# Kernel tuning notes

Hardware: AMD Instinct MI355X
Metric: run time of the kernel (lower is better)

Reference implementation:

```python
import jax, jax.numpy as jnp
import numpy as np

B, N, E = 2, 50000, 800000
F_IN, H1, C1, C2 = 1433, 8, 8, 7
NEG_SLOPE = 0.2
EPS = 1e-16


def _gat_conv(x, edge_index, W, a_src, a_dst, b, heads, out_ch):
    # x: [N, F_in]; edge_index: [2, E] (row0 = source j, row1 = target i, PyG convention)
    n = x.shape[0]
    loops = jnp.arange(n)
    src = jnp.concatenate([edge_index[0], loops])  # add self-loops (PyG default)
    dst = jnp.concatenate([edge_index[1], loops])
    h = (x @ W).reshape(n, heads, out_ch)                       # [N, H, C]
    e_src = (h * a_src).sum(-1)                                 # [N, H]
    e_dst = (h * a_dst).sum(-1)                                 # [N, H]
    e = jax.nn.leaky_relu(e_src[src] + e_dst[dst], NEG_SLOPE)   # [E', H]
    # segment softmax over incoming edges of each destination node
    m = jax.ops.segment_max(e, dst, num_segments=n)             # [N, H]
    ex = jnp.exp(e - m[dst])
    den = jax.ops.segment_sum(ex, dst, num_segments=n)
    alpha = ex / (den[dst] + EPS)                               # [E', H]
    out = jax.ops.segment_sum(h[src] * alpha[:, :, None], dst, num_segments=n)  # [N, H, C]
    return out.reshape(n, heads * out_ch) + b


def setup_inputs() -> dict:
    key = jax.random.key(0)
    ks = jax.random.split(key, 8)
    x = jax.random.normal(ks[0], (B, N, F_IN), dtype=jnp.float32)
    edge_index = jax.random.randint(ks[1], (B, 2, E), 0, N, dtype=jnp.int64)
    s1 = 1.0 / np.sqrt(F_IN)
    s2 = 1.0 / np.sqrt(H1 * C1)
    return {
        "x": x,
        "edge_index": edge_index,
        "W1": jax.random.normal(ks[2], (F_IN, H1 * C1), dtype=jnp.float32) * s1,
        "a1_src": jax.random.normal(ks[3], (H1, C1), dtype=jnp.float32) * 0.3,
        "a1_dst": jax.random.normal(ks[4], (H1, C1), dtype=jnp.float32) * 0.3,
        "b1": jnp.zeros((H1 * C1,), dtype=jnp.float32),
        "W2": jax.random.normal(ks[5], (H1 * C1, C2), dtype=jnp.float32) * s2,
        "a2_src": jax.random.normal(ks[6], (1, C2), dtype=jnp.float32) * 0.3,
        "a2_dst": jax.random.normal(ks[7], (1, C2), dtype=jnp.float32) * 0.3,
        "b2": jnp.zeros((C2,), dtype=jnp.float32),
    }


def reference(x, edge_index, W1, a1_src, a1_dst, b1, W2, a2_src, a2_dst, b2):
    # Eval mode: dropout (p=0.6) is identity.
    def per_graph(xi, ei):
        h = _gat_conv(xi, ei, W1, a1_src, a1_dst, b1, H1, C1)   # [N, 64]
        h = jax.nn.elu(h)
        o = _gat_conv(h, ei, W2, a2_src, a2_dst, b2, 1, C2)     # [N, 7]
        return jax.nn.log_softmax(o, axis=-1)
    return jax.vmap(per_graph)(x, edge_index)
```

## Files before the change

kernel.cpp:

```cpp
#include <hip/hip_runtime.h>
#include <hip/hip_bf16.h>
#include <math.h>

#define NB 2
#define NN 50000
#define NE 800000
#define FIN 1433
#define KPAD 1440
#define HD 64
#define C2c 7
#define NCHUNK 196

typedef __attribute__((ext_vector_type(8))) short short8;
typedef __attribute__((ext_vector_type(4))) float f32x4;
typedef f32x4 __attribute__((aligned(4))) f32x4u;

static __device__ __forceinline__ float leaky(float e) { return e > 0.f ? e : 0.2f * e; }

static __device__ __forceinline__ short bf16r(float f) {
    __hip_bfloat16 h = __float2bfloat16(f);
    return *reinterpret_cast<short*>(&h);
}

__global__ __launch_bounds__(256) void w1t_kernel(const float* __restrict__ W,
                                                  short* __restrict__ Bt) {
    int i = blockIdx.x * 256 + threadIdx.x;
    if (i >= 64 * KPAD) return;
    int c = i / KPAD, k = i - c * KPAD;
    float v = (k < FIN) ? W[k * 64 + c] : 0.f;
    Bt[i] = bf16r(v);
}

__global__ __launch_bounds__(256) void gemm1_mfma(const float* __restrict__ x,
                                                  const short* __restrict__ Bt,
                                                  float* __restrict__ h1) {
    const int b = blockIdx.y;
    const int wave = threadIdx.x >> 6;
    const int lane = threadIdx.x & 63;
    const int m = lane & 15;
    const int quad = lane >> 4;
    const int row0 = blockIdx.x * 128 + wave * 32;

    const float* xb = x + (size_t)b * NN * FIN;
    float* hb = h1 + (size_t)b * NN * HD;

    int r0 = row0 + m;
    int r1 = row0 + 16 + m;
    int r0c = r0 < NN ? r0 : NN - 1;
    int r1c = r1 < NN ? r1 : NN - 1;
    const float* a0p = xb + (size_t)r0c * FIN + quad * 8;
    const float* a1p = xb + (size_t)r1c * FIN + quad * 8;
    const short* btp = Bt + quad * 8 + (size_t)m * KPAD;

    f32x4 acc[2][4];
#pragma unroll
    for (int t = 0; t < 2; t++)
#pragma unroll
        for (int n = 0; n < 4; n++) acc[t][n] = (f32x4){0.f, 0.f, 0.f, 0.f};

    for (int kt = 0; kt < 1408; kt += 32) {
        f32x4 af00 = *(const f32x4u*)(a0p + kt);
        f32x4 af01 = *(const f32x4u*)(a0p + kt + 4);
        f32x4 af10 = *(const f32x4u*)(a1p + kt);
        f32x4 af11 = *(const f32x4u*)(a1p + kt + 4);
        short8 fa0, fa1;
        fa0[0] = bf16r(af00[0]); fa0[1] = bf16r(af00[1]); fa0[2] = bf16r(af00[2]); fa0[3] = bf16r(af00[3]);
        fa0[4] = bf16r(af01[0]); fa0[5] = bf16r(af01[1]); fa0[6] = bf16r(af01[2]); fa0[7] = bf16r(af01[3]);
        fa1[0] = bf16r(af10[0]); fa1[1] = bf16r(af10[1]); fa1[2] = bf16r(af10[2]); fa1[3] = bf16r(af10[3]);
        fa1[4] = bf16r(af11[0]); fa1[5] = bf16r(af11[1]); fa1[6] = bf16r(af11[2]); fa1[7] = bf16r(af11[3]);
#pragma unroll
        for (int n = 0; n < 4; n++) {
            short8 fb = *(const short8*)(btp + (size_t)n * 16 * KPAD + kt);
            acc[0][n] = __builtin_amdgcn_mfma_f32_16x16x32_bf16(fa0, fb, acc[0][n], 0, 0, 0);
            acc[1][n] = __builtin_amdgcn_mfma_f32_16x16x32_bf16(fa1, fb, acc[1][n], 0, 0, 0);
        }
    }
    {
        short8 fa0, fa1;
#pragma unroll
        for (int j = 0; j < 8; j++) {
            int k = 1408 + quad * 8 + j;
            fa0[j] = bf16r(k < FIN ? a0p[1408 + j] : 0.f);
            fa1[j] = bf16r(k < FIN ? a1p[1408 + j] : 0.f);
        }
#pragma unroll
        for (int n = 0; n < 4; n++) {
            short8 fb = *(const short8*)(btp + (size_t)n * 16 * KPAD + 1408);
            acc[0][n] = __builtin_amdgcn_mfma_f32_16x16x32_bf16(fa0, fb, acc[0][n], 0, 0, 0);
            acc[1][n] = __builtin_amdgcn_mfma_f32_16x16x32_bf16(fa1, fb, acc[1][n], 0, 0, 0);
        }
    }
#pragma unroll
    for (int t = 0; t < 2; t++) {
#pragma unroll
        for (int r = 0; r < 4; r++) {
            int row = row0 + t * 16 + quad * 4 + r;
            if (row < NN) {
#pragma unroll
                for (int n = 0; n < 4; n++) hb[(size_t)row * HD + n * 16 + m] = acc[t][n][r];
            }
        }
    }
}

__global__ void coef1_kernel(const float* __restrict__ h1, const float* __restrict__ a_src,
                             const float* __restrict__ a_dst, float* __restrict__ es,
                             float* __restrict__ ed) {
    int i = blockIdx.x * blockDim.x + threadIdx.x;
    if (i >= NB * NN * 8) return;
    int h = i & 7;
    int n = i >> 3;
    const float* hp = h1 + (size_t)n * 64 + h * 8;
    float s = 0.f, d = 0.f;
#pragma unroll
    for (int c = 0; c < 8; c++) {
        float v = hp[c];
        s += v * a_src[h * 8 + c];
        d += v * a_dst[h * 8 + c];
    }
    es[i] = s;
    ed[i] = d;
}

__global__ void deg_kernel(const int* __restrict__ ei, int* __restrict__ deg) {
    int i = blockIdx.x * blockDim.x + threadIdx.x;
    if (i >= NB * NE) return;
    int b = i / NE, e = i - b * NE;
    int dst = ei[(size_t)b * 2 * NE + NE + e];
    atomicAdd(deg + b * NN + dst, 1);
}

__global__ __launch_bounds__(256) void scan1_kernel(const int* __restrict__ deg,
                                                    int* __restrict__ rowptr,
                                                    int* __restrict__ bsum) {
    const int b = blockIdx.y, th = threadIdx.x;
    const int i = blockIdx.x * 256 + th;
    __shared__ int s[256];
    int v = (i < NN) ? deg[b * NN + i] : 0;
    s[th] = v;
    __syncthreads();
    int val = v;
    for (int off = 1; off < 256; off <<= 1) {
        int t = (th >= off) ? s[th - off] : 0;
        __syncthreads();
        val += t;
        s[th] = val;
        __syncthreads();
    }
    if (i < NN) rowptr[b * (NN + 1) + i] = val - v;
    if (th == 255) bsum[b * NCHUNK + blockIdx.x] = val;
}

__global__ __launch_bounds__(256) void scan2_kernel(const int* __restrict__ bsum,
                                                    int* __restrict__ boff,
                                                    int* __restrict__ rowptr) {
    const int b = blockIdx.x, th = threadIdx.x;
    __shared__ int s[256];
    int v = (th < NCHUNK) ? bsum[b * NCHUNK + th] : 0;
    s[th] = v;
    __syncthreads();
    int val = v;
    for (int off = 1; off < 256; off <<= 1) {
        int t = (th >= off) ? s[th - off] : 0;
        __syncthreads();
        val += t;
        s[th] = val;
        __syncthreads();
    }
    if (th < NCHUNK) boff[b * NCHUNK + th] = val - v;
    if (th == 255) rowptr[b * (NN + 1) + NN] = val;
}

__global__ __launch_bounds__(256) void scan3_kernel(const int* __restrict__ boff,
                                                    int* __restrict__ rowptr,
                                                    int* __restrict__ cursor) {
    const int b = blockIdx.y;
    const int i = blockIdx.x * 256 + threadIdx.x;
    if (i >= NN) return;
    int r = rowptr[b * (NN + 1) + i] + boff[b * NCHUNK + blockIdx.x];
    rowptr[b * (NN + 1) + i] = r;
    cursor[b * NN + i] = r;
}

__global__ void scatter_kernel(const int* __restrict__ ei, int* __restrict__ cursor,
                               int* __restrict__ col) {
    int i = blockIdx.x * blockDim.x + threadIdx.x;
    if (i >= NB * NE) return;
    int b = i / NE, e = i - b * NE;
    int src = ei[(size_t)b * 2 * NE + e];
    int dst = ei[(size_t)b * 2 * NE + NE + e];
    int pos = atomicAdd(cursor + b * NN + dst, 1);
    col[(size_t)b * NE + pos] = src;
}

__global__ __launch_bounds__(256) void agg1_kernel(
    const float* __restrict__ h1, const float* __restrict__ es, const float* __restrict__ ed,
    const float* __restrict__ b1, const float* __restrict__ W2, const float* __restrict__ a2s,
    const float* __restrict__ a2d, const int* __restrict__ rowptr, const int* __restrict__ col,
    float* __restrict__ h2, float* __restrict__ es2, float* __restrict__ ed2) {
    int w = blockIdx.x * 4 + (threadIdx.x >> 6);
    if (w >= NB * NN) return;
    const int lane = threadIdx.x & 63;
    const int b = w / NN;
    const int n = w - b * NN;
    const int head = lane >> 3;
    const size_t nb = (size_t)b * NN;

    const float edv = ed[(nb + n) * 8 + head];
    float accv = 0.f, den = 0.f;
    {
        float e = leaky(es[(nb + n) * 8 + head] + edv);
        float wv = __expf(e);
        den += wv;
        accv += wv * h1[(nb + n) * 64 + lane];
    }
    const int* cp = col + (size_t)b * NE;
    const int start = rowptr[b * (NN + 1) + n];
    const int end = rowptr[b * (NN + 1) + n + 1];
    for (int idx = start; idx < end; idx++) {
        int src = cp[idx];
        float e = leaky(es[(nb + src) * 8 + head] + edv);
        float wv = __expf(e);
        den += wv;
        accv += wv * h1[(nb + src) * 64 + lane];
    }
    float o = accv / (den + 1e-16f) + b1[lane];
    float g = o > 0.f ? o : expm1f(o);

    float h2reg = 0.f;
#pragma unroll
    for (int c2 = 0; c2 < 7; c2++) {
        float v = g * W2[lane * 7 + c2];
#pragma unroll
        for (int off = 1; off < 64; off <<= 1) v += __shfl_xor(v, off, 64);
        if (lane == c2) h2reg = v;
    }
    if (lane < 8) h2[(nb + n) * 8 + lane] = (lane < 7) ? h2reg : 0.f;

    float p = (lane < 7) ? h2reg * a2s[lane] : 0.f;
#pragma unroll
    for (int off = 1; off < 64; off <<= 1) p += __shfl_xor(p, off, 64);
    float q = (lane < 7) ? h2reg * a2d[lane] : 0.f;
#pragma unroll
    for (int off = 1; off < 64; off <<= 1) q += __shfl_xor(q, off, 64);
    if (lane == 0) {
        es2[nb + n] = p;
        ed2[nb + n] = q;
    }
}

__global__ void agg2_kernel(const float* __restrict__ h2, const float* __restrict__ es2,
                            const float* __restrict__ ed2, const float* __restrict__ b2,
                            const int* __restrict__ rowptr, const int* __restrict__ col,
                            float* __restrict__ out) {
    int i = blockIdx.x * blockDim.x + threadIdx.x;
    if (i >= NB * NN) return;
    const int b = i / NN;
    const int n = i - b * NN;
    const size_t nb = (size_t)b * NN;
    const float edv = ed2[nb + n];
    float acc0 = 0, acc1 = 0, acc2 = 0, acc3 = 0, acc4 = 0, acc5 = 0, acc6 = 0, den = 0;
    {
        float e = leaky(es2[nb + n] + edv);
        float wv = __expf(e);
        den += wv;
        const float4 u0 = *(const float4*)&h2[(nb + n) * 8];
        const float4 u1 = *(const float4*)&h2[(nb + n) * 8 + 4];
        acc0 += wv * u0.x; acc1 += wv * u0.y; acc2 += wv * u0.z; acc3 += wv * u0.w;
        acc4 += wv * u1.x; acc5 += wv * u1.y; acc6 += wv * u1.z;
    }
    const int* cp = col + (size_t)b * NE;
    const int start = rowptr[b * (NN + 1) + n];
    const int end = rowptr[b * (NN + 1) + n + 1];
    for (int idx = start; idx < end; idx++) {
        int src = cp[idx];
        float e = leaky(es2[nb + src] + edv);
        float wv = __expf(e);
        den += wv;
        const float4 u0 = *(const float4*)&h2[(nb + src) * 8];
        const float4 u1 = *(const float4*)&h2[(nb + src) * 8 + 4];
        acc0 += wv * u0.x; acc1 += wv * u0.y; acc2 += wv * u0.z; acc3 += wv * u0.w;
        acc4 += wv * u1.x; acc5 += wv * u1.y; acc6 += wv * u1.z;
    }
    float inv = 1.f / (den + 1e-16f);
    float o[7];
    o[0] = acc0 * inv + b2[0]; o[1] = acc1 * inv + b2[1]; o[2] = acc2 * inv + b2[2];
    o[3] = acc3 * inv + b2[3]; o[4] = acc4 * inv + b2[4]; o[5] = acc5 * inv + b2[5];
    o[6] = acc6 * inv + b2[6];
    float m = o[0];
#pragma unroll
    for (int c = 1; c < 7; c++) m = fmaxf(m, o[c]);
    float s = 0.f;
#pragma unroll
    for (int c = 0; c < 7; c++) s += expf(o[c] - m);
    float lse = m + logf(s);
    float* op = out + ((size_t)b * NN + n) * 7;
#pragma unroll
    for (int c = 0; c < 7; c++) op[c] = o[c] - lse;
}

extern "C" void kernel_launch(void* const* d_in, const int* in_sizes, int n_in,
                              void* d_out, int out_size, void* d_ws, size_t ws_size,
                              hipStream_t stream) {
    const float* x = (const float*)d_in[0];
    const int* ei = (const int*)d_in[1];
    const float* W1 = (const float*)d_in[2];
    const float* a1s = (const float*)d_in[3];
    const float* a1d = (const float*)d_in[4];
    const float* b1 = (const float*)d_in[5];
    const float* W2 = (const float*)d_in[6];
    const float* a2s = (const float*)d_in[7];
    const float* a2d = (const float*)d_in[8];
    const float* b2 = (const float*)d_in[9];
    float* out = (float*)d_out;

    char* ws = (char*)d_ws;
    size_t off = 0;
    auto alloc = [&](size_t bytes) {
        void* p = ws + off;
        off += (bytes + 255) & ~(size_t)255;
        return p;
    };
    float* h1 = (float*)alloc((size_t)NB * NN * 64 * 4);
    float* es1 = (float*)alloc((size_t)NB * NN * 8 * 4);
    float* ed1 = (float*)alloc((size_t)NB * NN * 8 * 4);
    float* h2 = (float*)alloc((size_t)NB * NN * 8 * 4);
    float* es2 = (float*)alloc((size_t)NB * NN * 4);
    float* ed2 = (float*)alloc((size_t)NB * NN * 4);
    int* rowptr = (int*)alloc((size_t)NB * (NN + 1) * 4);
    int* cursor = (int*)alloc((size_t)NB * NN * 4);
    int* deg = (int*)alloc((size_t)NB * NN * 4);
    int* col = (int*)alloc((size_t)NB * NE * 4);
    short* Bt = (short*)alloc((size_t)64 * KPAD * 2);
    int* bsum = (int*)alloc((size_t)NB * NCHUNK * 4);
    int* boff = (int*)alloc((size_t)NB * NCHUNK * 4);

    hipMemsetAsync(deg, 0, (size_t)NB * NN * 4, stream);

    w1t_kernel<<<(64 * KPAD + 255) / 256, 256, 0, stream>>>(W1, Bt);

    dim3 ggrid((NN + 127) / 128, NB);
    gemm1_mfma<<<ggrid, 256, 0, stream>>>(x, Bt, h1);

    coef1_kernel<<<(NB * NN * 8 + 255) / 256, 256, 0, stream>>>(h1, a1s, a1d, es1, ed1);

    deg_kernel<<<(NB * NE + 255) / 256, 256, 0, stream>>>(ei, deg);
    dim3 sgrid(NCHUNK, NB);
    scan1_kernel<<<sgrid, 256, 0, stream>>>(deg, rowptr, bsum);
    scan2_kernel<<<NB, 256, 0, stream>>>(bsum, boff, rowptr);
    scan3_kernel<<<sgrid, 256, 0, stream>>>(boff, rowptr, cursor);
    scatter_kernel<<<(NB * NE + 255) / 256, 256, 0, stream>>>(ei, cursor, col);

    agg1_kernel<<<(NB * NN + 3) / 4, 256, 0, stream>>>(h1, es1, ed1, b1, W2, a2s, a2d,
                                                       rowptr, col, h2, es2, ed2);
    agg2_kernel<<<(NB * NN + 255) / 256, 256, 0, stream>>>(h2, es2, ed2, b2, rowptr, col, out);
}
```

Measured before the change: 1.243 ms.

## Store layer-1 features as bf16 and parallelize agg1 across edges per wave

The GEMM output h1 is now stored as bf16 instead of fp32, which halves the bytes gathered per neighbor in coef1 and agg1. agg1 is restructured so that each wave's 8 lane-groups process different edges in parallel, with each lane owning one head's 8 channels via a 16-byte load. Partial sums are combined with cross-lane shuffles, and the W2 projection is reduced over 8 lanes instead of 64. This shortens the serial per-edge loop and lowers gather traffic, at the cost of bf16 rounding of the hidden features.

```diff
diff --git a/kernel.cpp b/kernel.cpp
--- a/kernel.cpp
+++ b/kernel.cpp
@@ -21,6 +21,10 @@
     __hip_bfloat16 h = __float2bfloat16(f);
     return *reinterpret_cast<short*>(&h);
 }
+static __device__ __forceinline__ float bf2f(short s) {
+    unsigned u = ((unsigned)(unsigned short)s) << 16;
+    return __uint_as_float(u);
+}
 
 __global__ __launch_bounds__(256) void w1t_kernel(const float* __restrict__ W,
                                                   short* __restrict__ Bt) {
@@ -33,7 +37,7 @@
 
 __global__ __launch_bounds__(256) void gemm1_mfma(const float* __restrict__ x,
                                                   const short* __restrict__ Bt,
-                                                  float* __restrict__ h1) {
+                                                  short* __restrict__ h1b) {
     const int b = blockIdx.y;
     const int wave = threadIdx.x >> 6;
     const int lane = threadIdx.x & 63;
@@ -42,7 +46,7 @@
     const int row0 = blockIdx.x * 128 + wave * 32;
 
     const float* xb = x + (size_t)b * NN * FIN;
-    float* hb = h1 + (size_t)b * NN * HD;
+    short* hb = h1b + (size_t)b * NN * HD;
 
     int r0 = row0 + m;
     int r1 = row0 + 16 + m;
@@ -97,24 +101,24 @@
             int row = row0 + t * 16 + quad * 4 + r;
             if (row < NN) {
 #pragma unroll
-                for (int n = 0; n < 4; n++) hb[(size_t)row * HD + n * 16 + m] = acc[t][n][r];
+                for (int n = 0; n < 4; n++) hb[(size_t)row * HD + n * 16 + m] = bf16r(acc[t][n][r]);
             }
         }
     }
 }
 
-__global__ void coef1_kernel(const float* __restrict__ h1, const float* __restrict__ a_src,
+__global__ void coef1_kernel(const short* __restrict__ h1b, const float* __restrict__ a_src,
                              const float* __restrict__ a_dst, float* __restrict__ es,
                              float* __restrict__ ed) {
     int i = blockIdx.x * blockDim.x + threadIdx.x;
     if (i >= NB * NN * 8) return;
     int h = i & 7;
     int n = i >> 3;
-    const float* hp = h1 + (size_t)n * 64 + h * 8;
+    const short8 hv = *(const short8*)(h1b + (size_t)n * 64 + h * 8);
     float s = 0.f, d = 0.f;
 #pragma unroll
     for (int c = 0; c < 8; c++) {
-        float v = hp[c];
+        float v = bf2f(hv[c]);
         s += v * a_src[h * 8 + c];
         d += v * a_dst[h * 8 + c];
     }
@@ -194,58 +198,88 @@
 }
 
 __global__ __launch_bounds__(256) void agg1_kernel(
-    const float* __restrict__ h1, const float* __restrict__ es, const float* __restrict__ ed,
+    const short* __restrict__ h1b, const float* __restrict__ es, const float* __restrict__ ed,
     const float* __restrict__ b1, const float* __restrict__ W2, const float* __restrict__ a2s,
     const float* __restrict__ a2d, const int* __restrict__ rowptr, const int* __restrict__ col,
     float* __restrict__ h2, float* __restrict__ es2, float* __restrict__ ed2) {
     int w = blockIdx.x * 4 + (threadIdx.x >> 6);
     if (w >= NB * NN) return;
     const int lane = threadIdx.x & 63;
+    const int s = lane >> 3;
+    const int cg = lane & 7;
     const int b = w / NN;
     const int n = w - b * NN;
-    const int head = lane >> 3;
     const size_t nb = (size_t)b * NN;
 
-    const float edv = ed[(nb + n) * 8 + head];
-    float accv = 0.f, den = 0.f;
-    {
-        float e = leaky(es[(nb + n) * 8 + head] + edv);
+    const float edv = ed[(nb + n) * 8 + cg];
+    float den = 0.f;
+    float acc[8];
+#pragma unroll
+    for (int j = 0; j < 8; j++) acc[j] = 0.f;
+
+    if (s == 0) {
+        float e = leaky(es[(nb + n) * 8 + cg] + edv);
         float wv = __expf(e);
-        den += wv;
-        accv += wv * h1[(nb + n) * 64 + lane];
-    }
+        den = wv;
+        const short8 hv = *(const short8*)(h1b + (nb + n) * 64 + cg * 8);
+#pragma unroll
+        for (int j = 0; j < 8; j++) acc[j] = wv * bf2f(hv[j]);
+    }
+
     const int* cp = col + (size_t)b * NE;
     const int start = rowptr[b * (NN + 1) + n];
     const int end = rowptr[b * (NN + 1) + n + 1];
-    for (int idx = start; idx < end; idx++) {
+    for (int idx = start + s; idx < end; idx += 8) {
         int src = cp[idx];
-        float e = leaky(es[(nb + src) * 8 + head] + edv);
+        float e = leaky(es[(nb + src) * 8 + cg] + edv);
         float wv = __expf(e);
         den += wv;
-        accv += wv * h1[(nb + src) * 64 + lane];
-    }
-    float o = accv / (den + 1e-16f) + b1[lane];
-    float g = o > 0.f ? o : expm1f(o);
-
-    float h2reg = 0.f;
+        const short8 hv = *(const short8*)(h1b + (nb + src) * 64 + cg * 8);
+#pragma unroll
+        for (int j = 0; j < 8; j++) acc[j] += wv * bf2f(hv[j]);
+    }
+
+#pragma unroll
+    for (int off = 8; off < 64; off <<= 1) {
+        den += __shfl_xor(den, off, 64);
+#pragma unroll
+        for (int j = 0; j < 8; j++) acc[j] += __shfl_xor(acc[j], off, 64);
+    }
+
+    const float inv = 1.f / (den + 1e-16f);
+    float g[8];
+#pragma unroll
+    for (int j = 0; j < 8; j++) {
+        float o = acc[j] * inv + b1[cg * 8 + j];
+        g[j] = o > 0.f ? o : expm1f(o);
+    }
+
+    float p[7];
 #pragma unroll
     for (int c2 = 0; c2 < 7; c2++) {
-        float v = g * W2[lane * 7 + c2];
-#pragma unroll
-        for (int off = 1; off < 64; off <<= 1) v += __shfl_xor(v, off, 64);
-        if (lane == c2) h2reg = v;
-    }
-    if (lane < 8) h2[(nb + n) * 8 + lane] = (lane < 7) ? h2reg : 0.f;
-
-    float p = (lane < 7) ? h2reg * a2s[lane] : 0.f;
-#pragma unroll
-    for (int off = 1; off < 64; off <<= 1) p += __shfl_xor(p, off, 64);
-    float q = (lane < 7) ? h2reg * a2d[lane] : 0.f;
-#pragma unroll
-    for (int off = 1; off < 64; off <<= 1) q += __shfl_xor(q, off, 64);
+        float v = 0.f;
+#pragma unroll
+        for (int j = 0; j < 8; j++) v += g[j] * W2[(cg * 8 + j) * 7 + c2];
+        p[c2] = v;
+    }
+#pragma unroll
+    for (int off = 1; off < 8; off <<= 1) {
+#pragma unroll
+        for (int c2 = 0; c2 < 7; c2++) p[c2] += __shfl_xor(p[c2], off, 64);
+    }
     if (lane == 0) {
-        es2[nb + n] = p;
-        ed2[nb + n] = q;
+        float4 v0 = make_float4(p[0], p[1], p[2], p[3]);
+        float4 v1 = make_float4(p[4], p[5], p[6], 0.f);
+        *(float4*)&h2[(nb + n) * 8] = v0;
+        *(float4*)&h2[(nb + n) * 8 + 4] = v1;
+        float s2 = 0.f, d2 = 0.f;
+#pragma unroll
+        for (int c2 = 0; c2 < 7; c2++) {
+            s2 += p[c2] * a2s[c2];
+            d2 += p[c2] * a2d[c2];
+        }
+        es2[nb + n] = s2;
+        ed2[nb + n] = d2;
     }
 }
 
@@ -290,10 +324,10 @@
     float m = o[0];
 #pragma unroll
     for (int c = 1; c < 7; c++) m = fmaxf(m, o[c]);
-    float s = 0.f;
-#pragma unroll
-    for (int c = 0; c < 7; c++) s += expf(o[c] - m);
-    float lse = m + logf(s);
+    float sum = 0.f;
+#pragma unroll
+    for (int c = 0; c < 7; c++) sum += expf(o[c] - m);
+    float lse = m + logf(sum);
     float* op = out + ((size_t)b * NN + n) * 7;
 #pragma unroll
     for (int c = 0; c < 7; c++) op[c] = o[c] - lse;
@@ -321,7 +355,7 @@
         off += (bytes + 255) & ~(size_t)255;
         return p;
     };
-    float* h1 = (float*)alloc((size_t)NB * NN * 64 * 4);
+    short* h1b = (short*)alloc((size_t)NB * NN * 64 * 2);
     float* es1 = (float*)alloc((size_t)NB * NN * 8 * 4);
     float* ed1 = (float*)alloc((size_t)NB * NN * 8 * 4);
     float* h2 = (float*)alloc((size_t)NB * NN * 8 * 4);
@@ -340,9 +374,9 @@
     w1t_kernel<<<(64 * KPAD + 255) / 256, 256, 0, stream>>>(W1, Bt);
 
     dim3 ggrid((NN + 127) / 128, NB);
-    gemm1_mfma<<<ggrid, 256, 0, stream>>>(x, Bt, h1);
-
-    coef1_kernel<<<(NB * NN * 8 + 255) / 256, 256, 0, stream>>>(h1, a1s, a1d, es1, ed1);
+    gemm1_mfma<<<ggrid, 256, 0, stream>>>(x, Bt, h1b);
+
+    coef1_kernel<<<(NB * NN * 8 + 255) / 256, 256, 0, stream>>>(h1b, a1s, a1d, es1, ed1);
 
     deg_kernel<<<(NB * NE + 255) / 256, 256, 0, stream>>>(ei, deg);
     dim3 sgrid(NCHUNK, NB);
@@ -351,7 +385,7 @@
     scan3_kernel<<<sgrid, 256, 0, stream>>>(boff, rowptr, cursor);
     scatter_kernel<<<(NB * NE + 255) / 256, 256, 0, stream>>>(ei, cursor, col);
 
-    agg1_kernel<<<(NB * NN + 3) / 4, 256, 0, stream>>>(h1, es1, ed1, b1, W2, a2s, a2d,
+    agg1_kernel<<<(NB * NN + 3) / 4, 256, 0, stream>>>(h1b, es1, ed1, b1, W2, a2s, a2d,
                                                        rowptr, col, h2, es2, ed2);
     agg2_kernel<<<(NB * NN + 255) / 256, 256, 0, stream>>>(h2, es2, ed2, b2, rowptr, col, out);
 }
```

Result: no change. 1.224 ms (-1.5%).
